# Performance work log

Hardware: AMD Instinct MI355X
Metric: run time of the kernel (lower is better)

## Reference

```python
import jax, jax.numpy as jnp
import numpy as np

B, L, H, E = 32, 256, 8, 16
SEQ_LEN = 64          # init seq_len, used only in final view
OUT = 256             # out_channels, must be divisible by SEQ_LEN
A = E + 1 + 128       # augmented channels: original + time + conv(128)
SIG_CH = A + A * A    # depth-2 signature channels
DN = ('NWC', 'WIO', 'NWC')


def setup_inputs() -> dict:
    key = jax.random.key(0)
    ks = jax.random.split(key, 8)
    return {
        'q': jax.random.normal(ks[0], (B, L, H, E), jnp.float32),
        'k': jax.random.normal(ks[1], (B, L, H, E), jnp.float32),
        'v': jax.random.normal(ks[2], (B, L, H, E), jnp.float32),
        'mask': jnp.zeros((B, L), jnp.bool_),
        'conv1_w': jax.random.normal(ks[3], (3, E, 64), jnp.float32) * 0.1,
        'conv1_b': jnp.zeros((64,), jnp.float32),
        'conv2_w': jax.random.normal(ks[4], (1, 64, 128), jnp.float32) * 0.1,
        'conv2_b': jnp.zeros((128,), jnp.float32),
        'lin_w': jax.random.normal(ks[5], (SIG_CH, OUT), jnp.float32) * 0.01,
        'lin_b': jnp.zeros((OUT,), jnp.float32),
    }


def _signature_depth2(p):
    # p: [N, S, C] piecewise-linear path. Returns [N, C + C*C].
    dx = p[:, 1:] - p[:, :-1]                       # [N, S-1, C]
    s1 = dx.sum(axis=1)                             # level 1
    cum_excl = jnp.cumsum(dx, axis=1) - dx          # sum of increments before t
    # level 2: sum_{s<t} dx_s (x) dx_t + 0.5 * dx_t (x) dx_t
    s2 = jnp.einsum('nti,ntj->nij', cum_excl + 0.5 * dx, dx)
    return jnp.concatenate([s1, s2.reshape(s2.shape[0], -1)], axis=-1)


def reference(q, k, v, mask, conv1_w, conv1_b, conv2_w, conv2_b, lin_w, lin_b):
    Bq, Lq, Hq, Eq = q.shape
    x = q.transpose(0, 2, 1, 3).reshape(Bq * Hq, Lq, Eq)   # [N, L, E]
    T = Lq - 3 + 1                                          # valid-conv length, kernel 3
    # Augment pieces
    trunc = x[:, 2:]                                        # [N, T, E]
    time = jnp.broadcast_to(jnp.linspace(0.0, 1.0, T, dtype=x.dtype)[None, :, None],
                            (Bq * Hq, T, 1))
    a = jax.lax.conv_general_dilated(x, conv1_w, (1,), 'VALID', dimension_numbers=DN) + conv1_b
    a = jax.nn.relu(jax.lax.conv_general_dilated(a, conv2_w, (1,), 'VALID', dimension_numbers=DN) + conv2_b)
    aug = jnp.concatenate([trunc, time, a], axis=2)         # [N, T, A]
    # lead-lag transform as written in source: interleave along time -> [N, 2T, A]
    lag = jnp.concatenate([aug[:, 1:], aug[:, -1:]], axis=1)
    ll = jnp.stack([aug, lag], axis=2).reshape(aug.shape[0], 2 * T, aug.shape[2])
    sig = _signature_depth2(ll)                             # [N, SIG_CH]
    out = sig @ lin_w + lin_b                               # [N, OUT]
    return out.reshape(Bq, Hq, SEQ_LEN, -1)
```

## Files before the change

kernel.cpp:

```cpp
#include <hip/hip_runtime.h>
#include <hip/hip_bf16.h>

#define Bq 32
#define Lq 256
#define Hq 8
#define Eq 16
#define Nn (Bq*Hq)
#define T 254
#define A 145
#define SIG_CH (A + A*A)
#define KP 21184
#define OUT 256

typedef __attribute__((ext_vector_type(8))) short short8;
typedef __attribute__((ext_vector_type(8))) unsigned short ushort8;
typedef __attribute__((ext_vector_type(4))) float floatx4;

static __device__ __forceinline__ unsigned short f2bf(float v) {
    unsigned int u = __float_as_uint(v);
    unsigned int r = (u + 0x7FFFu + ((u >> 16) & 1u)) >> 16;
    return (unsigned short)r;
}
static __device__ __forceinline__ float bf2f(unsigned short b) {
    return __uint_as_float(((unsigned int)b) << 16);
}

__global__ __launch_bounds__(256) void wprep_kernel(
    const float* __restrict__ W,
    unsigned short* __restrict__ wt_hi, unsigned short* __restrict__ wt_lo,
    const float* __restrict__ w1, const float* __restrict__ w2,
    unsigned short* __restrict__ w1im_hi, unsigned short* __restrict__ w1im_lo,
    unsigned short* __restrict__ w2t_hi,  unsigned short* __restrict__ w2t_lo)
{
    const int tid = threadIdx.x;
    if (blockIdx.x >= 1324) {
        int idx = (blockIdx.x - 1324)*256 + tid;
        if (idx < 4096) {
            int c = idx & 63, k = idx >> 6;
            float v = (k < 48) ? w1[k*64 + c] : 0.f;
            unsigned short hb = f2bf(v);
            w1im_hi[c*64 + k] = hb;
            w1im_lo[c*64 + k] = f2bf(v - bf2f(hb));
        } else {
            int j = idx - 4096;
            int c = j & 127, i = j >> 7;
            float v = w2[i*128 + c];
            unsigned short hb = f2bf(v);
            w2t_hi[c*64 + i] = hb;
            w2t_lo[c*64 + i] = f2bf(v - bf2f(hb));
        }
        return;
    }

    __shared__ float ls[64][65];
    const int k0 = (blockIdx.x % 331) * 64;
    const int o0 = (blockIdx.x / 331) * 64;

    #pragma unroll
    for (int p = 0; p < 16; ++p) {
        int idx = tid + p*256;
        int kk = idx >> 6, oo = idx & 63;
        int k = k0 + kk;
        ls[kk][oo] = (k < SIG_CH) ? W[(long)k*OUT + o0 + oo] : 0.f;
    }
    __syncthreads();

    const int oo = tid >> 2;
    const int kq = (tid & 3) * 16;
    unsigned short hbuf[16], lbuf[16];
    #pragma unroll
    for (int j = 0; j < 16; ++j) {
        float v = ls[kq + j][oo];
        unsigned short hb = f2bf(v);
        hbuf[j] = hb;
        lbuf[j] = f2bf(v - bf2f(hb));
    }
    long off = (long)(o0 + oo)*KP + k0 + kq;
    *(ushort8*)(wt_hi + off)     = *(ushort8*)&hbuf[0];
    *(ushort8*)(wt_hi + off + 8) = *(ushort8*)&hbuf[8];
    *(ushort8*)(wt_lo + off)     = *(ushort8*)&lbuf[0];
    *(ushort8*)(wt_lo + off + 8) = *(ushort8*)&lbuf[8];
}

#define MDS 40
#define OS3 36
#define XIS 72
#define GRPB 61600

__global__ __launch_bounds__(512) void augsig_kernel(
    const float* __restrict__ q,
    const float* __restrict__ b1, const float* __restrict__ b2,
    const unsigned short* __restrict__ w1im_hi, const unsigned short* __restrict__ w1im_lo,
    const unsigned short* __restrict__ w2t_hi,  const unsigned short* __restrict__ w2t_lo,
    unsigned short* __restrict__ sig_hi, unsigned short* __restrict__ sig_lo)
{
    __shared__ __align__(16) char smem[2*GRPB + 256 + 512 + 640 + 640];

    const int tid512 = threadIdx.x;
    const int grp = tid512 >> 8;
    const int tid = tid512 & 255;

    char* gb = smem + grp*GRPB;
    unsigned short* mdb = (unsigned short*)gb;
    float* outs = (float*)(gb + 38400);
    float* xsc  = (float*)(gb + 59280);
    float* b1s  = (float*)(smem + 2*GRPB);
    float* b2s  = b1s + 64;
    float* a0s  = b2s + 128;
    float* vls  = a0s + 160;
    float* accs = (float*)smem;

    unsigned short* Mh = mdb;
    unsigned short* Ml = mdb + 160*MDS;
    unsigned short* Dh = mdb + 2*160*MDS;
    unsigned short* ximh = mdb;
    unsigned short* ximl = mdb + 3456;
    unsigned short* a1h  = mdb + 6912;
    unsigned short* a1l  = mdb + 10368;

    const int n = blockIdx.x;
    const int b = n >> 3, h = n & 7;

    const int lane = tid & 63;
    const int wv   = tid >> 6;
    const int frow = lane & 15;
    const int quad = lane >> 4;
    const int wm = wv & 1, wn = wv >> 1;

    if (tid512 < 64)  b1s[tid512] = b1[tid512];
    if (tid512 < 128) b2s[tid512] = b2[tid512];

    const float4* q4 = (const float4*)q + ((long)(b*Lq)*Hq + h)*4;
    const float inv253 = 1.0f / 253.0f;

    float4 rq0, rq1, rq2, rq3;
    if (tid < 140) {
        const int r = tid >> 2, e4 = tid & 3;
        int t;
        t = (0*2 + grp)*32 + r; if (t > 255) t = 255; rq0 = q4[t*32 + e4];
        t = (1*2 + grp)*32 + r; if (t > 255) t = 255; rq1 = q4[t*32 + e4];
        t = (2*2 + grp)*32 + r; if (t > 255) t = 255; rq2 = q4[t*32 + e4];
        t = (3*2 + grp)*32 + r; if (t > 255) t = 255; rq3 = q4[t*32 + e4];
    }

    floatx4 acc[5][5];
    #pragma unroll
    for (int i = 0; i < 5; ++i)
        #pragma unroll
        for (int j = 0; j < 5; ++j)
            acc[i][j] = (floatx4){0.f, 0.f, 0.f, 0.f};

    #pragma unroll 1
    for (int ci = 0; ci < 4; ++ci) {
        const int c = 2*ci + grp;
        const int t0 = c*32;

        if (tid < 140) {
            float4 qv = (ci == 0) ? rq0 : (ci == 1) ? rq1 : (ci == 2) ? rq2 : rq3;
            ((float4*)xsc)[tid] = qv;
        }
        __syncthreads();

        for (int idx = tid; idx < 48*8; idx += 256) {
            int r = idx >> 3, g = idx & 7;
            unsigned short hh[8], ll[8];
            if (r <= 32 && g < 6) {
                const float* src = &xsc[r*16 + g*8];
                #pragma unroll
                for (int e = 0; e < 8; ++e) {
                    float v = src[e];
                    unsigned short hbv = f2bf(v);
                    hh[e] = hbv; ll[e] = f2bf(v - bf2f(hbv));
                }
            } else {
                #pragma unroll
                for (int e = 0; e < 8; ++e) { hh[e] = 0; ll[e] = 0; }
            }
            *(ushort8*)&ximh[r*XIS + g*8] = *(ushort8*)hh;
            *(ushort8*)&ximl[r*XIS + g*8] = *(ushort8*)ll;
        }
        __syncthreads();

        {
            short8 ah[3][2], al[3][2];
            #pragma unroll
            for (int mt = 0; mt < 3; ++mt)
                #pragma unroll
                for (int ks = 0; ks < 2; ++ks) {
                    int ar = (mt*16 + frow)*XIS + ks*32 + quad*8;
                    ah[mt][ks] = *(const short8*)&ximh[ar];
                    al[mt][ks] = *(const short8*)&ximl[ar];
                }
            short8 bh[2], bl[2];
            #pragma unroll
            for (int ks = 0; ks < 2; ++ks) {
                int br = (wv*16 + frow)*64 + ks*32 + quad*8;
                bh[ks] = *(const short8*)(w1im_hi + br);
                bl[ks] = *(const short8*)(w1im_lo + br);
            }
            floatx4 acc1[3];
            #pragma unroll
            for (int mt = 0; mt < 3; ++mt) acc1[mt] = (floatx4){0.f,0.f,0.f,0.f};
            #pragma unroll
            for (int mt = 0; mt < 3; ++mt)
                #pragma unroll
                for (int ks = 0; ks < 2; ++ks) {
                    acc1[mt] = __builtin_amdgcn_mfma_f32_16x16x32_bf16(ah[mt][ks], bh[ks], acc1[mt], 0,0,0);
                    acc1[mt] = __builtin_amdgcn_mfma_f32_16x16x32_bf16(ah[mt][ks], bl[ks], acc1[mt], 0,0,0);
                    acc1[mt] = __builtin_amdgcn_mfma_f32_16x16x32_bf16(al[mt][ks], bh[ks], acc1[mt], 0,0,0);
                }
            const int cc = wv*16 + frow;
            const float bias = b1s[cc];
            #pragma unroll
            for (int mt = 0; mt < 3; ++mt)
                #pragma unroll
                for (int e = 0; e < 4; ++e) {
                    int t = mt*16 + quad*4 + e;
                    float v = acc1[mt][e] + bias;
                    unsigned short hbv = f2bf(v);
                    a1h[t*XIS + cc] = hbv;
                    a1l[t*XIS + cc] = f2bf(v - bf2f(hbv));
                }
        }
        __syncthreads();

        {
            short8 ah[3][2], al[3][2];
            #pragma unroll
            for (int mt = 0; mt < 3; ++mt)
                #pragma unroll
                for (int ks = 0; ks < 2; ++ks) {
                    int ar = (mt*16 + frow)*XIS + ks*32 + quad*8;
                    ah[mt][ks] = *(const short8*)&a1h[ar];
                    al[mt][ks] = *(const short8*)&a1l[ar];
                }
            short8 bh[2][2], bl[2][2];
            #pragma unroll
            for (int nt = 0; nt < 2; ++nt)
                #pragma unroll
                for (int ks = 0; ks < 2; ++ks) {
                    int br = (wv*32 + nt*16 + frow)*64 + ks*32 + quad*8;
                    bh[nt][ks] = *(const short8*)(w2t_hi + br);
                    bl[nt][ks] = *(const short8*)(w2t_lo + br);
                }
            floatx4 acc2[3][2];
            #pragma unroll
            for (int mt = 0; mt < 3; ++mt)
                #pragma unroll
                for (int nt = 0; nt < 2; ++nt)
                    acc2[mt][nt] = (floatx4){0.f,0.f,0.f,0.f};
            #pragma unroll
            for (int mt = 0; mt < 3; ++mt)
                #pragma unroll
                for (int nt = 0; nt < 2; ++nt)
                    #pragma unroll
                    for (int ks = 0; ks < 2; ++ks) {
                        acc2[mt][nt] = __builtin_amdgcn_mfma_f32_16x16x32_bf16(ah[mt][ks], bh[nt][ks], acc2[mt][nt], 0,0,0);
                        acc2[mt][nt] = __builtin_amdgcn_mfma_f32_16x16x32_bf16(ah[mt][ks], bl[nt][ks], acc2[mt][nt], 0,0,0);
                        acc2[mt][nt] = __builtin_amdgcn_mfma_f32_16x16x32_bf16(al[mt][ks], bh[nt][ks], acc2[mt][nt], 0,0,0);
                    }
            #pragma unroll
            for (int mt = 0; mt < 3; ++mt)
                #pragma unroll
                for (int nt = 0; nt < 2; ++nt) {
                    int cc = wv*32 + nt*16 + frow;
                    float bias = b2s[cc];
                    int tb = mt*16 + quad*4;
                    if (tb <= 32) {
                        float4 vv;
                        vv.x = fmaxf(acc2[mt][nt][0] + bias, 0.f);
                        vv.y = fmaxf(acc2[mt][nt][1] + bias, 0.f);
                        vv.z = fmaxf(acc2[mt][nt][2] + bias, 0.f);
                        vv.w = fmaxf(acc2[mt][nt][3] + bias, 0.f);
                        *(float4*)&outs[(17 + cc)*OS3 + tb] = vv;
                    }
                }
        }
        for (int idx = tid; idx < 17*33; idx += 256) {
            int ch = idx / 33, tt = idx - ch*33;
            float val = (ch < 16) ? xsc[(tt+2)*16 + ch] : (float)(t0+tt)*inv253;
            outs[ch*OS3 + tt] = val;
        }
        __syncthreads();

        for (int task = tid; task < 290; task += 256) {
            int ch = task >> 1, hh2 = task & 1;
            const float* orow = &outs[ch*OS3 + hh2*16];
            float v[17];
            float4 va = *(const float4*)&orow[0];
            float4 vb = *(const float4*)&orow[4];
            float4 vc = *(const float4*)&orow[8];
            float4 vd = *(const float4*)&orow[12];
            v[0]=va.x; v[1]=va.y; v[2]=va.z; v[3]=va.w;
            v[4]=vb.x; v[5]=vb.y; v[6]=vb.z; v[7]=vb.w;
            v[8]=vc.x; v[9]=vc.y; v[10]=vc.z; v[11]=vc.w;
            v[12]=vd.x; v[13]=vd.y; v[14]=vd.z; v[15]=vd.w;
            v[16] = orow[16];
            if (c == 0 && hh2 == 0) a0s[ch] = v[0];
            if (c == 7 && hh2 == 1) vls[ch] = v[13];
            unsigned short mh[16], ml[16], dh[16];
            const int tbase = t0 + hh2*16;
            #pragma unroll
            for (int tl = 0; tl < 16; ++tl) {
                bool valid = (tbase + tl) <= 252;
                float x0 = v[tl], x1 = v[tl+1];
                float d = valid ? (x1 - x0) : 0.f;
                float m = valid ? (0.5f*(x0 + x1)) : 0.f;
                unsigned short hbv = f2bf(m);
                mh[tl] = hbv; ml[tl] = f2bf(m - bf2f(hbv));
                dh[tl] = f2bf(d);
            }
            int mo = ch*MDS + hh2*16;
            *(ushort8*)&Mh[mo]     = *(ushort8*)&mh[0];
            *(ushort8*)&Mh[mo + 8] = *(ushort8*)&mh[8];
            *(ushort8*)&Ml[mo]     = *(ushort8*)&ml[0];
            *(ushort8*)&Ml[mo + 8] = *(ushort8*)&ml[8];
            *(ushort8*)&Dh[mo]     = *(ushort8*)&dh[0];
            *(ushort8*)&Dh[mo + 8] = *(ushort8*)&dh[8];
        }
        __syncthreads();

        {
            short8 afh[5], afl[5], bfh[5];
            #pragma unroll
            for (int i = 0; i < 5; ++i) {
                int ar = (wm*80 + i*16 + frow)*MDS + quad*8;
                int br = (wn*80 + i*16 + frow)*MDS + quad*8;
                afh[i] = *(const short8*)&Mh[ar];
                afl[i] = *(const short8*)&Ml[ar];
                bfh[i] = *(const short8*)&Dh[br];
            }
            #pragma unroll
            for (int mt = 0; mt < 5; ++mt)
                #pragma unroll
                for (int nt = 0; nt < 5; ++nt) {
                    acc[mt][nt] = __builtin_amdgcn_mfma_f32_16x16x32_bf16(
                        afh[mt], bfh[nt], acc[mt][nt], 0, 0, 0);
                    acc[mt][nt] = __builtin_amdgcn_mfma_f32_16x16x32_bf16(
                        afl[mt], bfh[nt], acc[mt][nt], 0, 0, 0);
                }
        }
    }

    __syncthreads();

    if (grp == 1) {
        #pragma unroll
        for (int mt = 0; mt < 5; ++mt)
            #pragma unroll
            for (int nt = 0; nt < 5; ++nt) {
                int j = wn*80 + nt*16 + frow;
                int ib = wm*80 + mt*16 + quad*4;
                #pragma unroll
                for (int e = 0; e < 4; ++e)
                    accs[(ib + e)*160 + j] = acc[mt][nt][e];
            }
    }
    __syncthreads();

    if (grp == 0) {
        #pragma unroll
        for (int mt = 0; mt < 5; ++mt)
            #pragma unroll
            for (int nt = 0; nt < 5; ++nt) {
                int j = wn*80 + nt*16 + frow;
                int ib = wm*80 + mt*16 + quad*4;
                float s1j = (j < A) ? (vls[j] - a0s[j]) : 0.f;
                #pragma unroll
                for (int e = 0; e < 4; ++e) {
                    int i = ib + e;
                    float a0i = (i < A) ? a0s[i] : 0.f;
                    accs[i*160 + j] = acc[mt][nt][e] + accs[i*160 + j] - a0i*s1j;
                }
            }
    }
    __syncthreads();

    unsigned short* sh = sig_hi + (long)n*KP;
    unsigned short* sl = sig_lo + (long)n*KP;

    if (tid512 < 290) {
        const int r = tid512 >> 1, hh2 = tid512 & 1;
        const float* row = accs + r*160;
        const long g0 = (long)A + (long)r*A;
        const int s0 = (8 - (int)(g0 & 7)) & 7;
        if (hh2 == 0) {
            for (int j = 0; j < s0; ++j) {
                float v = row[j];
                unsigned short hbv = f2bf(v);
                sh[g0 + j] = hbv;
                sl[g0 + j] = f2bf(v - bf2f(hbv));
            }
            for (int vb8 = 0; vb8 < 8; ++vb8) {
                int j0 = s0 + vb8*8;
                unsigned short hb8[8], lb8[8];
                #pragma unroll
                for (int e = 0; e < 8; ++e) {
                    float v = row[j0 + e];
                    unsigned short hbv = f2bf(v);
                    hb8[e] = hbv; lb8[e] = f2bf(v - bf2f(hbv));
                }
                *(ushort8*)(sh + g0 + j0) = *(ushort8*)hb8;
                *(ushort8*)(sl + g0 + j0) = *(ushort8*)lb8;
            }
        } else {
            int j0 = s0 + 64;
            for (; j0 + 8 <= A; j0 += 8) {
                unsigned short hb8[8], lb8[8];
                #pragma unroll
                for (int e = 0; e < 8; ++e) {
                    float v = row[j0 + e];
                    unsigned short hbv = f2bf(v);
                    hb8[e] = hbv; lb8[e] = f2bf(v - bf2f(hbv));
                }
                *(ushort8*)(sh + g0 + j0) = *(ushort8*)hb8;
                *(ushort8*)(sl + g0 + j0) = *(ushort8*)lb8;
            }
            for (; j0 < A; ++j0) {
                float v = row[j0];
                unsigned short hbv = f2bf(v);
                sh[g0 + j0] = hbv;
                sl[g0 + j0] = f2bf(v - bf2f(hbv));
            }
        }
    } else if (tid512 < 290 + A) {
        int ch = tid512 - 290;
        float v = vls[ch] - a0s[ch];
        unsigned short hbv = f2bf(v);
        sh[ch] = hbv;
        sl[ch] = f2bf(v - bf2f(hbv));
    } else if (tid512 < 290 + A + (KP - SIG_CH)) {
        int p = tid512 - (290 + A);
        sh[SIG_CH + p] = 0;
        sl[SIG_CH + p] = 0;
    }
}

#define SPLITK 61
#define KC 352
#define NSTEP (KC/32)
#define LDA 40

__global__ __launch_bounds__(256) void gemm_kernel(
    const unsigned short* __restrict__ sig_hi, const unsigned short* __restrict__ sig_lo,
    const unsigned short* __restrict__ wt_hi,  const unsigned short* __restrict__ wt_lo,
    float* __restrict__ part)
{
    __shared__ __align__(16) unsigned short Ah[128*LDA];
    __shared__ __align__(16) unsigned short Al[128*LDA];
    __shared__ __align__(16) unsigned short Bh[64*LDA];
    __shared__ __align__(16) unsigned short Bl[64*LDA];

    const int tid = threadIdx.x;
    const int lin  = blockIdx.x + 4*blockIdx.y + 8*blockIdx.z;
    const int lin2 = (lin & 7)*61 + (lin >> 3);
    const int z  = lin2 >> 3;
    const int m  = lin2 & 7;
    const int o0 = (m & 3) * 64;
    const int n0 = (m >> 2) * 128;
    const int k0 = z * KC;

    const int lane = tid & 63;
    const int w    = tid >> 6;
    const int wm   = w & 1;
    const int wn   = w >> 1;
    const int frow = lane & 15;
    const int quad = lane >> 4;

    const int srowA = tid >> 1;
    const int khA   = (tid & 1) * 16;
    const int srowB = tid >> 2;
    const int kqB   = (tid & 3) * 8;

    const unsigned short* gAh = sig_hi + (long)(n0 + srowA)*KP;
    const unsigned short* gAl = sig_lo + (long)(n0 + srowA)*KP;
    const unsigned short* gBh = wt_hi  + (long)(o0 + srowB)*KP;
    const unsigned short* gBl = wt_lo  + (long)(o0 + srowB)*KP;

    ushort8 rah[2], ral[2], rbh, rbl;
    const ushort8 z8 = {0,0,0,0,0,0,0,0};

    #define GLOAD(s)                                                          \
        {                                                                     \
            int kb = k0 + (s)*32;                                             \
            if (kb < KP) {                                                    \
                rah[0] = *(const ushort8*)(gAh + kb + khA);                   \
                rah[1] = *(const ushort8*)(gAh + kb + khA + 8);               \
                ral[0] = *(const ushort8*)(gAl + kb + khA);                   \
                ral[1] = *(const ushort8*)(gAl + kb + khA + 8);               \
                rbh    = *(const ushort8*)(gBh + kb + kqB);                   \
                rbl    = *(const ushort8*)(gBl + kb + kqB);                   \
            } else {                                                          \
                rah[0]=z8; rah[1]=z8; ral[0]=z8; ral[1]=z8;                   \
                rbh=z8; rbl=z8;                                               \
            }                                                                 \
        }

    #define LSTORE()                                                          \
        {                                                                     \
            int oA = srowA*LDA + khA;                                         \
            *(ushort8*)(Ah + oA)     = rah[0];                                \
            *(ushort8*)(Ah + oA + 8) = rah[1];                                \
            *(ushort8*)(Al + oA)     = ral[0];                                \
            *(ushort8*)(Al + oA + 8) = ral[1];                                \
            int oB = srowB*LDA + kqB;                                         \
            *(ushort8*)(Bh + oB) = rbh;                                       \
            *(ushort8*)(Bl + oB) = rbl;                                       \
        }

    floatx4 acc[4][2];
    #pragma unroll
    for (int i = 0; i < 4; ++i)
        #pragma unroll
        for (int j = 0; j < 2; ++j)
            acc[i][j] = (floatx4){0.f, 0.f, 0.f, 0.f};

    GLOAD(0);
    LSTORE();
    __syncthreads();

    for (int s = 0; s < NSTEP; ++s) {
        if (s < NSTEP-1) GLOAD(s+1);

        short8 afh[4], afl[4], bfh[2], bfl[2];
        const int aoff = (wm*64 + frow)*LDA + quad*8;
        const int boff = (wn*32 + frow)*LDA + quad*8;
        #pragma unroll
        for (int tI = 0; tI < 4; ++tI) {
            afh[tI] = *(const short8*)(Ah + aoff + tI*16*LDA);
            afl[tI] = *(const short8*)(Al + aoff + tI*16*LDA);
        }
        #pragma unroll
        for (int tI = 0; tI < 2; ++tI) {
            bfh[tI] = *(const short8*)(Bh + boff + tI*16*LDA);
            bfl[tI] = *(const short8*)(Bl + boff + tI*16*LDA);
        }
        #pragma unroll
        for (int mt = 0; mt < 4; ++mt)
            #pragma unroll
            for (int nt = 0; nt < 2; ++nt) {
                acc[mt][nt] = __builtin_amdgcn_mfma_f32_16x16x32_bf16(
                    afh[mt], bfh[nt], acc[mt][nt], 0, 0, 0);
                acc[mt][nt] = __builtin_amdgcn_mfma_f32_16x16x32_bf16(
                    afh[mt], bfl[nt], acc[mt][nt], 0, 0, 0);
                acc[mt][nt] = __builtin_amdgcn_mfma_f32_16x16x32_bf16(
                    afl[mt], bfh[nt], acc[mt][nt], 0, 0, 0);
            }
        __syncthreads();
        if (s < NSTEP-1) {
            LSTORE();
            __syncthreads();
        }
    }

    float* pz = part + (long)z * (Nn*OUT);
    #pragma unroll
    for (int mt = 0; mt < 4; ++mt)
        #pragma unroll
        for (int nt = 0; nt < 2; ++nt) {
            int col = o0 + wn*32 + nt*16 + frow;
            int rbase = n0 + wm*64 + mt*16 + quad*4;
            #pragma unroll
            for (int e = 0; e < 4; ++e)
                pz[(long)(rbase + e)*OUT + col] = acc[mt][nt][e];
        }
}

__global__ __launch_bounds__(256) void reduce_kernel(
    const float* __restrict__ part, const float* __restrict__ lb,
    float* __restrict__ out)
{
    int idx = blockIdx.x * 256 + threadIdx.x;
    float s = lb[idx & 255];
    #pragma unroll 8
    for (int z = 0; z < SPLITK; ++z)
        s += part[(long)z * (Nn*OUT) + idx];
    out[idx] = s;
}

extern "C" void kernel_launch(void* const* d_in, const int* in_sizes, int n_in,
                              void* d_out, int out_size, void* d_ws, size_t ws_size,
                              hipStream_t stream) {
    const float* q  = (const float*)d_in[0];
    const float* w1 = (const float*)d_in[4];
    const float* b1 = (const float*)d_in[5];
    const float* w2 = (const float*)d_in[6];
    const float* b2 = (const float*)d_in[7];
    const float* lw = (const float*)d_in[8];
    const float* lb = (const float*)d_in[9];
    float* out = (float*)d_out;

    char* ws = (char*)d_ws;
    unsigned short* sig_hi  = (unsigned short*)ws;
    unsigned short* sig_lo  = (unsigned short*)(ws + 10846208);
    unsigned short* wt_hi   = (unsigned short*)(ws + 21692416);
    unsigned short* wt_lo   = (unsigned short*)(ws + 32538624);
    float*          part    = (float*)(ws + 43384832);
    unsigned short* w1im_hi = (unsigned short*)(ws + 43384832);
    unsigned short* w1im_lo = (unsigned short*)(ws + 43384832 + 8192);
    unsigned short* w2t_hi  = (unsigned short*)(ws + 43384832 + 16384);
    unsigned short* w2t_lo  = (unsigned short*)(ws + 43384832 + 32768);

    wprep_kernel<<<1372, 256, 0, stream>>>(lw, wt_hi, wt_lo,
                                           w1, w2, w1im_hi, w1im_lo, w2t_hi, w2t_lo);
    augsig_kernel<<<Nn, 512, 0, stream>>>(q, b1, b2, w1im_hi, w1im_lo, w2t_hi, w2t_lo, sig_hi, sig_lo);
    gemm_kernel<<<dim3(4, 2, SPLITK), 256, 0, stream>>>(sig_hi, sig_lo, wt_hi, wt_lo, part);
    reduce_kernel<<<(Nn*OUT)/256, 256, 0, stream>>>(part, lb, out);
}
```

Measured before the change: 157.6 us.

## Fuse linear-weight bf16 split into GEMM loads and pad accumulator stride

Drops the separate pass that transposed and split the 21K×256 linear weight into hi/lo bf16 buffers. The GEMM now reads fp32 weights directly, with coalesced loads across output columns, and does the hi/lo split in registers before storing to shared memory. This removes a full write and re-read of roughly 21 MB of intermediate weights, at the cost of redundant conversion per block and strided per-k loads. The shared-memory accumulator row stride also changes from 160 to 162, which is meant to reduce LDS bank conflicts.

```diff
diff --git a/kernel.cpp b/kernel.cpp
--- a/kernel.cpp
+++ b/kernel.cpp
@@ -26,66 +26,32 @@
 }
 
 __global__ __launch_bounds__(256) void wprep_kernel(
-    const float* __restrict__ W,
-    unsigned short* __restrict__ wt_hi, unsigned short* __restrict__ wt_lo,
     const float* __restrict__ w1, const float* __restrict__ w2,
     unsigned short* __restrict__ w1im_hi, unsigned short* __restrict__ w1im_lo,
     unsigned short* __restrict__ w2t_hi,  unsigned short* __restrict__ w2t_lo)
 {
-    const int tid = threadIdx.x;
-    if (blockIdx.x >= 1324) {
-        int idx = (blockIdx.x - 1324)*256 + tid;
-        if (idx < 4096) {
-            int c = idx & 63, k = idx >> 6;
-            float v = (k < 48) ? w1[k*64 + c] : 0.f;
-            unsigned short hb = f2bf(v);
-            w1im_hi[c*64 + k] = hb;
-            w1im_lo[c*64 + k] = f2bf(v - bf2f(hb));
-        } else {
-            int j = idx - 4096;
-            int c = j & 127, i = j >> 7;
-            float v = w2[i*128 + c];
-            unsigned short hb = f2bf(v);
-            w2t_hi[c*64 + i] = hb;
-            w2t_lo[c*64 + i] = f2bf(v - bf2f(hb));
-        }
-        return;
-    }
-
-    __shared__ float ls[64][65];
-    const int k0 = (blockIdx.x % 331) * 64;
-    const int o0 = (blockIdx.x / 331) * 64;
-
-    #pragma unroll
-    for (int p = 0; p < 16; ++p) {
-        int idx = tid + p*256;
-        int kk = idx >> 6, oo = idx & 63;
-        int k = k0 + kk;
-        ls[kk][oo] = (k < SIG_CH) ? W[(long)k*OUT + o0 + oo] : 0.f;
-    }
-    __syncthreads();
-
-    const int oo = tid >> 2;
-    const int kq = (tid & 3) * 16;
-    unsigned short hbuf[16], lbuf[16];
-    #pragma unroll
-    for (int j = 0; j < 16; ++j) {
-        float v = ls[kq + j][oo];
+    int idx = blockIdx.x*256 + threadIdx.x;
+    if (idx < 4096) {
+        int c = idx & 63, k = idx >> 6;
+        float v = (k < 48) ? w1[k*64 + c] : 0.f;
         unsigned short hb = f2bf(v);
-        hbuf[j] = hb;
-        lbuf[j] = f2bf(v - bf2f(hb));
-    }
-    long off = (long)(o0 + oo)*KP + k0 + kq;
-    *(ushort8*)(wt_hi + off)     = *(ushort8*)&hbuf[0];
-    *(ushort8*)(wt_hi + off + 8) = *(ushort8*)&hbuf[8];
-    *(ushort8*)(wt_lo + off)     = *(ushort8*)&lbuf[0];
-    *(ushort8*)(wt_lo + off + 8) = *(ushort8*)&lbuf[8];
+        w1im_hi[c*64 + k] = hb;
+        w1im_lo[c*64 + k] = f2bf(v - bf2f(hb));
+    } else {
+        int j = idx - 4096;
+        int c = j & 127, i = j >> 7;
+        float v = w2[i*128 + c];
+        unsigned short hb = f2bf(v);
+        w2t_hi[c*64 + i] = hb;
+        w2t_lo[c*64 + i] = f2bf(v - bf2f(hb));
+    }
 }
 
 #define MDS 40
 #define OS3 36
 #define XIS 72
 #define GRPB 61600
+#define ACS 162
 
 __global__ __launch_bounds__(512) void augsig_kernel(
     const float* __restrict__ q,
@@ -353,7 +319,7 @@
                 int ib = wm*80 + mt*16 + quad*4;
                 #pragma unroll
                 for (int e = 0; e < 4; ++e)
-                    accs[(ib + e)*160 + j] = acc[mt][nt][e];
+                    accs[(ib + e)*ACS + j] = acc[mt][nt][e];
             }
     }
     __syncthreads();
@@ -370,7 +336,7 @@
                 for (int e = 0; e < 4; ++e) {
                     int i = ib + e;
                     float a0i = (i < A) ? a0s[i] : 0.f;
-                    accs[i*160 + j] = acc[mt][nt][e] + accs[i*160 + j] - a0i*s1j;
+                    accs[i*ACS + j] = acc[mt][nt][e] + accs[i*ACS + j] - a0i*s1j;
                 }
             }
     }
@@ -381,7 +347,7 @@
 
     if (tid512 < 290) {
         const int r = tid512 >> 1, hh2 = tid512 & 1;
-        const float* row = accs + r*160;
+        const float* row = accs + r*ACS;
         const long g0 = (long)A + (long)r*A;
         const int s0 = (8 - (int)(g0 & 7)) & 7;
         if (hh2 == 0) {
@@ -443,7 +409,7 @@
 
 __global__ __launch_bounds__(256) void gemm_kernel(
     const unsigned short* __restrict__ sig_hi, const unsigned short* __restrict__ sig_lo,
-    const unsigned short* __restrict__ wt_hi,  const unsigned short* __restrict__ wt_lo,
+    const float* __restrict__ W,
     float* __restrict__ part)
 {
     __shared__ __align__(16) unsigned short Ah[128*LDA];
@@ -469,15 +435,15 @@
 
     const int srowA = tid >> 1;
     const int khA   = (tid & 1) * 16;
-    const int srowB = tid >> 2;
-    const int kqB   = (tid & 3) * 8;
+    const int oo    = tid & 63;
+    const int ks8   = tid >> 6;
 
     const unsigned short* gAh = sig_hi + (long)(n0 + srowA)*KP;
     const unsigned short* gAl = sig_lo + (long)(n0 + srowA)*KP;
-    const unsigned short* gBh = wt_hi  + (long)(o0 + srowB)*KP;
-    const unsigned short* gBl = wt_lo  + (long)(o0 + srowB)*KP;
-
-    ushort8 rah[2], ral[2], rbh, rbl;
+    const float*          gB  = W + (o0 + oo);
+
+    ushort8 rah[2], ral[2];
+    float wv8[8];
     const ushort8 z8 = {0,0,0,0,0,0,0,0};
 
     #define GLOAD(s)                                                          \
@@ -488,11 +454,14 @@
                 rah[1] = *(const ushort8*)(gAh + kb + khA + 8);               \
                 ral[0] = *(const ushort8*)(gAl + kb + khA);                   \
                 ral[1] = *(const ushort8*)(gAl + kb + khA + 8);               \
-                rbh    = *(const ushort8*)(gBh + kb + kqB);                   \
-                rbl    = *(const ushort8*)(gBl + kb + kqB);                   \
             } else {                                                          \
                 rah[0]=z8; rah[1]=z8; ral[0]=z8; ral[1]=z8;                   \
-                rbh=z8; rbl=z8;                                               \
+            }                                                                 \
+            int kbb = kb + ks8*8;                                             \
+            _Pragma("unroll")                                                 \
+            for (int j = 0; j < 8; ++j) {                                     \
+                int k = kbb + j;                                              \
+                wv8[j] = (k < SIG_CH) ? gB[(long)k*OUT] : 0.f;                \
             }                                                                 \
         }
 
@@ -503,9 +472,15 @@
             *(ushort8*)(Ah + oA + 8) = rah[1];                                \
             *(ushort8*)(Al + oA)     = ral[0];                                \
             *(ushort8*)(Al + oA + 8) = ral[1];                                \
-            int oB = srowB*LDA + kqB;                                         \
-            *(ushort8*)(Bh + oB) = rbh;                                       \
-            *(ushort8*)(Bl + oB) = rbl;                                       \
+            unsigned short hb8[8], lb8[8];                                    \
+            _Pragma("unroll")                                                 \
+            for (int j = 0; j < 8; ++j) {                                     \
+                unsigned short hbv = f2bf(wv8[j]);                            \
+                hb8[j] = hbv; lb8[j] = f2bf(wv8[j] - bf2f(hbv));              \
+            }                                                                 \
+            int oB = oo*LDA + ks8*8;                                          \
+            *(ushort8*)(Bh + oB) = *(ushort8*)hb8;                            \
+            *(ushort8*)(Bl + oB) = *(ushort8*)lb8;                            \
         }
 
     floatx4 acc[4][2];
@@ -593,17 +568,14 @@
     char* ws = (char*)d_ws;
     unsigned short* sig_hi  = (unsigned short*)ws;
     unsigned short* sig_lo  = (unsigned short*)(ws + 10846208);
-    unsigned short* wt_hi   = (unsigned short*)(ws + 21692416);
-    unsigned short* wt_lo   = (unsigned short*)(ws + 32538624);
     float*          part    = (float*)(ws + 43384832);
     unsigned short* w1im_hi = (unsigned short*)(ws + 43384832);
     unsigned short* w1im_lo = (unsigned short*)(ws + 43384832 + 8192);
     unsigned short* w2t_hi  = (unsigned short*)(ws + 43384832 + 16384);
     unsigned short* w2t_lo  = (unsigned short*)(ws + 43384832 + 32768);
 
-    wprep_kernel<<<1372, 256, 0, stream>>>(lw, wt_hi, wt_lo,
-                                           w1, w2, w1im_hi, w1im_lo, w2t_hi, w2t_lo);
+    wprep_kernel<<<48, 256, 0, stream>>>(w1, w2, w1im_hi, w1im_lo, w2t_hi, w2t_lo);
     augsig_kernel<<<Nn, 512, 0, stream>>>(q, b1, b2, w1im_hi, w1im_lo, w2t_hi, w2t_lo, sig_hi, sig_lo);
-    gemm_kernel<<<dim3(4, 2, SPLITK), 256, 0, stream>>>(sig_hi, sig_lo, wt_hi, wt_lo, part);
+    gemm_kernel<<<dim3(4, 2, SPLITK), 256, 0, stream>>>(sig_hi, sig_lo, lw, part);
     reduce_kernel<<<(Nn*OUT)/256, 256, 0, stream>>>(part, lb, out);
 }
```

New measurement: 153.1 us. -2.9%, faster.
